# Optimization experiments

Hardware: AMD Instinct MI355X
Metric: run time of the kernel (lower is better)

The kernel has to match this reference:

```python
import jax, jax.numpy as jnp
import numpy as np

K = 501   # box-filter length (conv kernel height)
P = 250   # reflect padding on each side of the time axis


def setup_inputs() -> dict:
    key = jax.random.key(0)
    k1, k2 = jax.random.split(key)
    pred = jax.random.normal(k1, (8, 16384, 128), dtype=jnp.float32)  # [B, T, C]
    # Conv2d default bias init: U(-b, b) with b = 1/sqrt(fan_in) = 1/sqrt(501)
    b = 1.0 / np.sqrt(K)
    bias = jax.random.uniform(k2, (1,), dtype=jnp.float32, minval=-b, maxval=b)
    return {"pred": pred, "bias": bias}


def reference(pred, bias):
    # Reflect-pad the time axis, then compute the 501-wide moving sum via a
    # prefix-sum (O(N) instead of O(N*K) dense conv) — same math as the
    # all-ones Conv2d kernel with reflect padding.
    x = jnp.pad(pred, ((0, 0), (P, P), (0, 0)), mode="reflect")  # [B, T+2P, C]
    c = jnp.cumsum(x, axis=1)
    c = jnp.concatenate([jnp.zeros_like(c[:, :1, :]), c], axis=1)  # [B, T+2P+1, C]
    win_sum = c[:, K:, :] - c[:, :-K, :]                            # [B, T, C]
    smoothed = (win_sum + bias[0]) / K  # conv output (ones weights + bias) / kernel_size
    return jnp.maximum(pred, smoothed)
```

## Files before the change

### kernel.cpp

```cpp
#include <hip/hip_runtime.h>


constexpr int B     = 8;
constexpr int T     = 16384;
constexpr int C     = 128;
constexpr int K     = 501;
constexpr int CHN   = 16;
constexpr int NCG   = C / CHN;
constexpr int NSEG  = 16;
constexpr int SEGR  = T / NSEG;
constexpr int CHK   = 32;
constexpr int RROWS = 576;
constexpr int RPAD  = 17;
constexpr int RSZ   = RROWS * RPAD;
constexpr int MARG  = 256;
constexpr int PRO   = 17;
constexpr int NCHK  = 48;

__device__ __forceinline__ int ridx(int j) {
    j = (j < 0) ? -j : j;
    return (j >= T) ? (2 * T - 2 - j) : j;
}

__global__ __launch_bounds__(256, 4) void smoother_kernel(
    const float* __restrict__ pred, const float* __restrict__ bias,
    float* __restrict__ out) {
    __shared__ float ring[RSZ];

    const int b   = blockIdx.x & 7;
    const int cg  = (blockIdx.x >> 3) & 7;
    const int seg = blockIdx.x >> 6;
    const int g0  = seg * SEGR;
    const int jstart = g0 - MARG;

    const int tid  = threadIdx.x;
    const int lane = tid & 63;
    const int w    = tid >> 6;
    const int rowq = lane >> 2;
    const int cs   = lane & 3;
    const int ch   = w * 4 + cs;

    const int srow = tid >> 3;
    const int chp  = tid & 7;

    const float* pb = pred + (size_t)b * T * C + cg * CHN;
    float*       ob = out  + (size_t)b * T * C + cg * CHN;

    const float rk  = 1.0f / (float)K;
    const float brk = bias[0] * rk;

    {
        float2 pv0[PRO];
        #pragma unroll
        for (int m = 0; m < PRO; ++m) {
            const int jr = ridx(jstart + m * CHK + srow);
            pv0[m] = *reinterpret_cast<const float2*>(
                pb + (size_t)jr * C + chp * 2);
        }
        #pragma unroll
        for (int m = 0; m < PRO; ++m) {
            const int p = m * CHK + srow;
            float* d = &ring[p * RPAD + chp * 2];
            d[0] = pv0[m].x; d[1] = pv0[m].y;
        }
    }
    __syncthreads();

    float acc = 0.0f;
    #pragma unroll 8
    for (int k2 = 0; k2 < 31; ++k2)
        acc += ring[(6 + rowq + 16 * k2) * RPAD + ch];
    if (rowq <= 4) acc += ring[(502 + rowq) * RPAD + ch];
    acc += __shfl_xor(acc, 4);
    acc += __shfl_xor(acc, 8);
    acc += __shfl_xor(acc, 16);
    acc += __shfl_xor(acc, 32);
    float S = acc;

    int idxn = (507 + rowq) * RPAD + ch;
    int idxo = (6   + rowq) * RPAD + ch;
    int idxc = (256 + rowq) * RPAD + ch;
    float* op = ob + (size_t)(g0 + rowq) * C + ch;

    int pm = PRO * CHK;
    float2 pv;

    for (int i = 0; i < SEGR / CHK; ++i) {
        const bool do_stage = (i + PRO) < NCHK;
        if (do_stage) {
            const int jr = ridx(jstart + (i + PRO) * CHK + srow);
            pv = *reinterpret_cast<const float2*>(
                pb + (size_t)jr * C + chp * 2);
        }

        #pragma unroll
        for (int s = 0; s < 2; ++s) {
            const float vn = ring[idxn];
            const float vo = ring[idxo];
            const float vc = ring[idxc];
            const float d  = vn - vo;
            float x = d;
            const float u1 = __shfl_up(x, 4);  if (lane >= 4)  x += u1;
            const float u2 = __shfl_up(x, 8);  if (lane >= 8)  x += u2;
            const float u3 = __shfl_up(x, 16); if (lane >= 16) x += u3;
            const float u4 = __shfl_up(x, 32); if (lane >= 32) x += u4;
            const float tot = __shfl(x, 60 + cs);
            const float sm  = S + (x - d);
            const float o   = fmaxf(vc, fmaf(sm, rk, brk));
            __builtin_nontemporal_store(o, op);
            S += tot;
            idxn += 16 * RPAD; if (idxn >= RSZ) idxn -= RSZ;
            idxo += 16 * RPAD; if (idxo >= RSZ) idxo -= RSZ;
            idxc += 16 * RPAD; if (idxc >= RSZ) idxc -= RSZ;
            op += 16 * C;
        }

        if (do_stage) {
            int p = pm + srow; if (p >= RROWS) p -= RROWS;
            float* d = &ring[p * RPAD + chp * 2];
            d[0] = pv.x; d[1] = pv.y;
            pm += CHK; if (pm >= RROWS) pm -= RROWS;
        }
        __syncthreads();
    }
}

extern "C" void kernel_launch(void* const* d_in, const int* in_sizes, int n_in,
                              void* d_out, int out_size, void* d_ws, size_t ws_size,
                              hipStream_t stream) {
    const float* pred = (const float*)d_in[0];
    const float* bias = (const float*)d_in[1];
    float*       out  = (float*)d_out;

    const int blocks = B * NCG * NSEG;
    smoother_kernel<<<blocks, 256, 0, stream>>>(pred, bias, out);
}
```

Baseline: 132.8 us.

## Store ring buffer in fp16 with swizzle, widen blocks to 32 channels and 512 threads

The shared ring buffer now holds fp16 instead of fp32, with an XOR-style slot swizzle replacing row padding to avoid bank conflicts. Each block covers 32 channels with 512 threads, and each lane does a 64-row scan over four channels using float4 loads and stores. The centre value is re-read from global memory in fp32. Storing window values in half precision lowers accuracy of the 501-wide running sum and risks tolerance failures; the change also adds an extra barrier per step.

Measured after the change: 207.6 us. +56.3%, slower.

```diff
diff --git a/kernel.cpp b/kernel.cpp
--- a/kernel.cpp
+++ b/kernel.cpp
@@ -1,47 +1,47 @@
 #include <hip/hip_runtime.h>
+#include <hip/hip_fp16.h>
 
 
 constexpr int B     = 8;
 constexpr int T     = 16384;
 constexpr int C     = 128;
 constexpr int K     = 501;
-constexpr int CHN   = 16;
+constexpr int CHN   = 32;
 constexpr int NCG   = C / CHN;
-constexpr int NSEG  = 16;
+constexpr int NSEG  = 32;
 constexpr int SEGR  = T / NSEG;
-constexpr int CHK   = 32;
-constexpr int RROWS = 576;
-constexpr int RPAD  = 17;
-constexpr int RSZ   = RROWS * RPAD;
+constexpr int STEP  = 64;
+constexpr int NSTEP = SEGR / STEP;
+constexpr int CHK   = 64;
+constexpr int RROWS = 640;
 constexpr int MARG  = 256;
-constexpr int PRO   = 17;
-constexpr int NCHK  = 48;
+constexpr int PRO   = 9;
+constexpr int NCHK  = 16;
 
 __device__ __forceinline__ int ridx(int j) {
     j = (j < 0) ? -j : j;
     return (j >= T) ? (2 * T - 2 - j) : j;
 }
 
-__global__ __launch_bounds__(256, 4) void smoother_kernel(
+typedef float f32x4 __attribute__((ext_vector_type(4)));
+
+__global__ __launch_bounds__(512, 8) void smoother_kernel(
     const float* __restrict__ pred, const float* __restrict__ bias,
     float* __restrict__ out) {
-    __shared__ float ring[RSZ];
+    __shared__ __align__(16) unsigned int ring[RROWS * 16];
 
     const int b   = blockIdx.x & 7;
-    const int cg  = (blockIdx.x >> 3) & 7;
-    const int seg = blockIdx.x >> 6;
+    const int cg  = (blockIdx.x >> 3) & (NCG - 1);
+    const int seg = blockIdx.x >> 5;
     const int g0  = seg * SEGR;
     const int jstart = g0 - MARG;
 
     const int tid  = threadIdx.x;
     const int lane = tid & 63;
     const int w    = tid >> 6;
-    const int rowq = lane >> 2;
-    const int cs   = lane & 3;
-    const int ch   = w * 4 + cs;
 
     const int srow = tid >> 3;
-    const int chp  = tid & 7;
+    const int sq   = tid & 7;
 
     const float* pb = pred + (size_t)b * T * C + cg * CHN;
     float*       ob = out  + (size_t)b * T * C + cg * CHN;
@@ -49,77 +49,115 @@
     const float rk  = 1.0f / (float)K;
     const float brk = bias[0] * rk;
 
-    {
-        float2 pv0[PRO];
-        #pragma unroll
-        for (int m = 0; m < PRO; ++m) {
-            const int jr = ridx(jstart + m * CHK + srow);
-            pv0[m] = *reinterpret_cast<const float2*>(
-                pb + (size_t)jr * C + chp * 2);
-        }
-        #pragma unroll
-        for (int m = 0; m < PRO; ++m) {
-            const int p = m * CHK + srow;
-            float* d = &ring[p * RPAD + chp * 2];
-            d[0] = pv0[m].x; d[1] = pv0[m].y;
-        }
+    #pragma unroll 3
+    for (int m = 0; m < PRO; ++m) {
+        const int jr = ridx(jstart + m * CHK + srow);
+        const float4 v = *reinterpret_cast<const float4*>(
+            pb + (size_t)jr * C + sq * 4);
+        const int p = m * CHK + srow;
+        __half2 h0 = __float22half2_rn(make_float2(v.x, v.y));
+        __half2 h1 = __float22half2_rn(make_float2(v.z, v.w));
+        const int slot = (sq + p + (p >> 3)) & 7;
+        unsigned int* d = &ring[p * 16 + slot * 2];
+        d[0] = *reinterpret_cast<unsigned int*>(&h0);
+        d[1] = *reinterpret_cast<unsigned int*>(&h1);
     }
     __syncthreads();
 
-    float acc = 0.0f;
-    #pragma unroll 8
-    for (int k2 = 0; k2 < 31; ++k2)
-        acc += ring[(6 + rowq + 16 * k2) * RPAD + ch];
-    if (rowq <= 4) acc += ring[(502 + rowq) * RPAD + ch];
-    acc += __shfl_xor(acc, 4);
-    acc += __shfl_xor(acc, 8);
-    acc += __shfl_xor(acc, 16);
-    acc += __shfl_xor(acc, 32);
-    float S = acc;
+    float Sx = 0.f, Sy = 0.f, Sz = 0.f, Sw = 0.f;
+    {
+        #pragma unroll
+        for (int k = 0; k < 7; ++k) {
+            const int p = 6 + lane + 64 * k;
+            const int slot = (w + p + (p >> 3)) & 7;
+            const uint2 v = *reinterpret_cast<const uint2*>(
+                &ring[p * 16 + slot * 2]);
+            const float2 lo = __half22float2(*reinterpret_cast<const __half2*>(&v.x));
+            const float2 hi = __half22float2(*reinterpret_cast<const __half2*>(&v.y));
+            Sx += lo.x; Sy += lo.y; Sz += hi.x; Sw += hi.y;
+        }
+        if (lane <= 52) {
+            const int p = 454 + lane;
+            const int slot = (w + p + (p >> 3)) & 7;
+            const uint2 v = *reinterpret_cast<const uint2*>(
+                &ring[p * 16 + slot * 2]);
+            const float2 lo = __half22float2(*reinterpret_cast<const __half2*>(&v.x));
+            const float2 hi = __half22float2(*reinterpret_cast<const __half2*>(&v.y));
+            Sx += lo.x; Sy += lo.y; Sz += hi.x; Sw += hi.y;
+        }
+        #pragma unroll
+        for (int d = 1; d <= 32; d <<= 1) {
+            Sx += __shfl_xor(Sx, d);
+            Sy += __shfl_xor(Sy, d);
+            Sz += __shfl_xor(Sz, d);
+            Sw += __shfl_xor(Sw, d);
+        }
+    }
 
-    int idxn = (507 + rowq) * RPAD + ch;
-    int idxo = (6   + rowq) * RPAD + ch;
-    int idxc = (256 + rowq) * RPAD + ch;
-    float* op = ob + (size_t)(g0 + rowq) * C + ch;
+    #pragma unroll 1
+    for (int i = 0; i < NSTEP; ++i) {
+        float4 sv;
+        int sp = 0;
+        const bool do_stage = (PRO + i) < NCHK;
+        if (do_stage) {
+            const int m  = PRO + i;
+            const int jr = ridx(jstart + m * CHK + srow);
+            sv = *reinterpret_cast<const float4*>(pb + (size_t)jr * C + sq * 4);
+            sp = m * CHK + srow; if (sp >= RROWS) sp -= RROWS;
+        }
+        const float4 cv = *reinterpret_cast<const float4*>(
+            pb + (size_t)(g0 + 64 * i + lane) * C + w * 4);
 
-    int pm = PRO * CHK;
-    float2 pv;
+        int pn = 507 + 64 * i + lane; if (pn >= RROWS) pn -= RROWS;
+        int po = 6   + 64 * i + lane;
+        const int sn = (w + pn + (pn >> 3)) & 7;
+        const int so = (w + po + (po >> 3)) & 7;
+        const uint2 un = *reinterpret_cast<const uint2*>(&ring[pn * 16 + sn * 2]);
+        const uint2 uo = *reinterpret_cast<const uint2*>(&ring[po * 16 + so * 2]);
+        const float2 nlo = __half22float2(*reinterpret_cast<const __half2*>(&un.x));
+        const float2 nhi = __half22float2(*reinterpret_cast<const __half2*>(&un.y));
+        const float2 olo = __half22float2(*reinterpret_cast<const __half2*>(&uo.x));
+        const float2 ohi = __half22float2(*reinterpret_cast<const __half2*>(&uo.y));
 
-    for (int i = 0; i < SEGR / CHK; ++i) {
-        const bool do_stage = (i + PRO) < NCHK;
-        if (do_stage) {
-            const int jr = ridx(jstart + (i + PRO) * CHK + srow);
-            pv = *reinterpret_cast<const float2*>(
-                pb + (size_t)jr * C + chp * 2);
+        const float dx = nlo.x - olo.x;
+        const float dy = nlo.y - olo.y;
+        const float dz = nhi.x - ohi.x;
+        const float dw = nhi.y - ohi.y;
+
+        float xx = dx, xy = dy, xz = dz, xw = dw;
+        #pragma unroll
+        for (int lvl = 0; lvl < 6; ++lvl) {
+            const int dd = 1 << lvl;
+            const float ux = __shfl_up(xx, dd);
+            const float uy = __shfl_up(xy, dd);
+            const float uz = __shfl_up(xz, dd);
+            const float uw = __shfl_up(xw, dd);
+            if (lane >= dd) { xx += ux; xy += uy; xz += uz; xw += uw; }
         }
+        const float totx = __shfl(xx, 63);
+        const float toty = __shfl(xy, 63);
+        const float totz = __shfl(xz, 63);
+        const float totw = __shfl(xw, 63);
 
-        #pragma unroll
-        for (int s = 0; s < 2; ++s) {
-            const float vn = ring[idxn];
-            const float vo = ring[idxo];
-            const float vc = ring[idxc];
-            const float d  = vn - vo;
-            float x = d;
-            const float u1 = __shfl_up(x, 4);  if (lane >= 4)  x += u1;
-            const float u2 = __shfl_up(x, 8);  if (lane >= 8)  x += u2;
-            const float u3 = __shfl_up(x, 16); if (lane >= 16) x += u3;
-            const float u4 = __shfl_up(x, 32); if (lane >= 32) x += u4;
-            const float tot = __shfl(x, 60 + cs);
-            const float sm  = S + (x - d);
-            const float o   = fmaxf(vc, fmaf(sm, rk, brk));
-            __builtin_nontemporal_store(o, op);
-            S += tot;
-            idxn += 16 * RPAD; if (idxn >= RSZ) idxn -= RSZ;
-            idxo += 16 * RPAD; if (idxo >= RSZ) idxo -= RSZ;
-            idxc += 16 * RPAD; if (idxc >= RSZ) idxc -= RSZ;
-            op += 16 * C;
-        }
+        f32x4 o;
+        o.x = fmaxf(cv.x, fmaf(Sx + (xx - dx), rk, brk));
+        o.y = fmaxf(cv.y, fmaf(Sy + (xy - dy), rk, brk));
+        o.z = fmaxf(cv.z, fmaf(Sz + (xz - dz), rk, brk));
+        o.w = fmaxf(cv.w, fmaf(Sw + (xw - dw), rk, brk));
+        __builtin_nontemporal_store(
+            o, reinterpret_cast<f32x4*>(ob + (size_t)(g0 + 64 * i + lane) * C + w * 4));
+
+        Sx += totx; Sy += toty; Sz += totz; Sw += totw;
+
+        __syncthreads();
 
         if (do_stage) {
-            int p = pm + srow; if (p >= RROWS) p -= RROWS;
-            float* d = &ring[p * RPAD + chp * 2];
-            d[0] = pv.x; d[1] = pv.y;
-            pm += CHK; if (pm >= RROWS) pm -= RROWS;
+            __half2 h0 = __float22half2_rn(make_float2(sv.x, sv.y));
+            __half2 h1 = __float22half2_rn(make_float2(sv.z, sv.w));
+            const int slot = (sq + sp + (sp >> 3)) & 7;
+            unsigned int* d = &ring[sp * 16 + slot * 2];
+            d[0] = *reinterpret_cast<unsigned int*>(&h0);
+            d[1] = *reinterpret_cast<unsigned int*>(&h1);
         }
         __syncthreads();
     }
@@ -133,5 +171,5 @@
     float*       out  = (float*)d_out;
 
     const int blocks = B * NCG * NSEG;
-    smoother_kernel<<<blocks, 256, 0, stream>>>(pred, bias, out);
+    smoother_kernel<<<blocks, 512, 0, stream>>>(pred, bias, out);
 }
```
